# Performance work log

Measured on AMD Instinct MI355X. Metric: run time of the kernel, lower is better.

The kernel has to match this reference:

```python
import jax, jax.numpy as jnp
import numpy as np

H = 128
IN = 5
EPS = 1e-5


def lstm(x, Wih, Whh, bih, bhh):
    # x: [B,T,D]; PyTorch gate order i,f,g,o along 4H axis
    B, T, _ = x.shape
    xW = jnp.einsum('btd,gd->btg', x, Wih) + bih + bhh  # [B,T,4H]
    WhhT = Whh.T

    def step(carry, xt):
        h, c = carry
        g = xt + h @ WhhT
        i, f, gg, o = jnp.split(g, 4, axis=-1)
        i = jax.nn.sigmoid(i)
        f = jax.nn.sigmoid(f)
        gg = jnp.tanh(gg)
        o = jax.nn.sigmoid(o)
        c = f * c + i * gg
        h = o * jnp.tanh(c)
        return (h, c), h

    h0 = jnp.zeros((B, H), x.dtype)
    _, hs = jax.lax.scan(step, (h0, h0), jnp.swapaxes(xW, 0, 1))
    return jnp.swapaxes(hs, 0, 1)  # [B,T,H]


def batchnorm(x, gamma, beta):
    # training-mode BN over (batch, time) per channel; x: [B,T,H]
    mean = jnp.mean(x, axis=(0, 1))
    var = jnp.var(x, axis=(0, 1))
    return (x - mean) * (gamma * jax.lax.rsqrt(var + EPS)) + beta


def forward_one(x, Wih1, Whh1, bih1, bhh1, g1, b1, Wih2, Whh2, bih2, bhh2, g2, b2, fcW, fcb):
    out = lstm(x, Wih1, Whh1, bih1, bhh1)
    out = batchnorm(out, g1, b1)
    # dropout is identity (eval / deterministic reference)
    out = lstm(out, Wih2, Whh2, bih2, bhh2)
    out = batchnorm(out, g2, b2)
    emb = out[:, -1, :] @ fcW.T + fcb  # [B,128]
    norm = jnp.sqrt(jnp.sum(emb * emb, axis=1, keepdims=True))
    return emb / jnp.maximum(norm, 1e-12)  # F.normalize p=2


def setup_inputs() -> dict:
    key = jax.random.key(0)
    ks = jax.random.split(key, 20)
    B, T = 512, 128
    s_in = 1.0 / np.sqrt(H)
    d = {
        'a': jax.random.normal(ks[0], (B, T, IN), jnp.float32),
        'p': jax.random.normal(ks[1], (B, T, IN), jnp.float32),
        'n': jax.random.normal(ks[2], (B, T, IN), jnp.float32),
        'Wih1': jax.random.uniform(ks[3], (4 * H, IN), jnp.float32, -s_in, s_in),
        'Whh1': jax.random.uniform(ks[4], (4 * H, H), jnp.float32, -s_in, s_in),
        'bih1': jax.random.uniform(ks[5], (4 * H,), jnp.float32, -s_in, s_in),
        'bhh1': jax.random.uniform(ks[6], (4 * H,), jnp.float32, -s_in, s_in),
        'g1': jnp.ones((H,), jnp.float32),
        'b1': jnp.zeros((H,), jnp.float32),
        'Wih2': jax.random.uniform(ks[7], (4 * H, H), jnp.float32, -s_in, s_in),
        'Whh2': jax.random.uniform(ks[8], (4 * H, H), jnp.float32, -s_in, s_in),
        'bih2': jax.random.uniform(ks[9], (4 * H,), jnp.float32, -s_in, s_in),
        'bhh2': jax.random.uniform(ks[10], (4 * H,), jnp.float32, -s_in, s_in),
        'g2': jnp.ones((H,), jnp.float32),
        'b2': jnp.zeros((H,), jnp.float32),
        'fcW': jax.random.uniform(ks[11], (H, H), jnp.float32, -s_in, s_in),
        'fcb': jax.random.uniform(ks[12], (H,), jnp.float32, -s_in, s_in),
    }
    return d


def reference(a, p, n, Wih1, Whh1, bih1, bhh1, g1, b1, Wih2, Whh2, bih2, bhh2, g2, b2, fcW, fcb):
    f = lambda x: forward_one(x, Wih1, Whh1, bih1, bhh1, g1, b1, Wih2, Whh2, bih2, bhh2, g2, b2, fcW, fcb)
    return (f(a), f(p), f(n))
```

## Files before the change

### kernel.cpp

```cpp
#include <hip/hip_runtime.h>


typedef __attribute__((ext_vector_type(8))) _Float16 half8;
typedef __attribute__((ext_vector_type(4))) float f32x4;

#define TS 128
#define HID 128
#define NGATE 512
#define INV_N (1.0f/65536.0f)
#define NL2E  -1.4426950408889634f
#define N2L2E -2.8853900817779268f
#define GCLAMP 57.707801635558536f

#define BAR() asm volatile("s_waitcnt lgkmcnt(0)\n\ts_barrier" ::: "memory")

__device__ __forceinline__ float rcpf(float x) { return __builtin_amdgcn_rcpf(x); }
__device__ __forceinline__ float ex2(float x) { return __builtin_amdgcn_exp2f(x); }

__device__ __forceinline__ float lstm_cell(float zi, float zf, float zg, float zo,
                                           float& c) {
  float zgc = __builtin_amdgcn_fmed3f(zg, -GCLAMP, GCLAMP);
  float ei = ex2(zi);
  float ef = ex2(zf);
  float eg = ex2(zgc);
  float eo = ex2(zo);
  float pi = 1.0f + ei, pg = 1.0f + eg, pf = 1.0f + ef;
  float P = pi * pg;
  float rd = rcpf(P * pf);
  float fv = P * rd;
  float ig = (1.0f - eg) * (pf * rd);
  float cc = fv * c + ig;
  c = cc;
  float t2 = __builtin_amdgcn_fmed3f(cc * N2L2E, -GCLAMP, GCLAMP);
  float ec = ex2(t2);
  float hv = (1.0f - ec) * rcpf((1.0f + eo) * (1.0f + ec));
  return hv;
}


__global__ void prep_all(const float* __restrict__ xa, const float* __restrict__ xp,
                         const float* __restrict__ xn,
                         const float* __restrict__ Whh1, const float* __restrict__ Whh2,
                         const float* __restrict__ bih1, const float* __restrict__ bhh1,
                         _Float16* __restrict__ xpad,
                         _Float16* __restrict__ whhT1, _Float16* __restrict__ whhT2,
                         float* __restrict__ b1c) {
  int bid = blockIdx.x, tid = threadIdx.x;
  if (bid < 768) {
    int i = bid * 256 + tid;
    int tile = i >> 11, rem = i & 2047;
    int t = rem >> 4, r = rem & 15;
    int inp = tile >> 5, rloc = (tile & 31) * 16;
    const float* x = (inp == 0) ? xa : ((inp == 1) ? xp : xn);
    const float* row = x + (size_t)(rloc + r) * 640 + t * 5;
    half8 v = {0, 0, 0, 0, 0, 0, 0, 0};
#pragma unroll
    for (int j = 0; j < 5; ++j) v[j] = (_Float16)row[j];
    *(half8*)&xpad[(size_t)i * 8] = v;
  } else if (bid < 832) {
    int i = (bid - 768) * 256 + tid;
    int which = i >> 13, i8 = i & 8191;
    int kq = i8 >> 9, g = i8 & 511;
    int k0 = (kq >> 2) * 32 + (kq & 3) * 8;
    float gs = ((g >> 7) == 2) ? N2L2E : NL2E;
    const float* src = which ? Whh2 : Whh1;
    half8 v;
#pragma unroll
    for (int j = 0; j < 8; ++j) v[j] = (_Float16)(src[(size_t)g * HID + k0 + j] * gs);
    *(half8*)&(which ? whhT2 : whhT1)[(size_t)i8 * 8] = v;
  } else {
    int i = (bid - 832) * 256 + tid;
    float gs = ((i >> 7) == 2) ? N2L2E : NL2E;
    b1c[i] = (bih1[i] + bhh1[i]) * gs;
  }
}

__global__ __launch_bounds__(512, 2) void lstm1_kernel(
    const _Float16* __restrict__ xpad,
    const float* __restrict__ Wih1,
    const float* __restrict__ b1c,
    const _Float16* __restrict__ whhT,
    _Float16* __restrict__ hs1,
    float* __restrict__ s1sum, float* __restrict__ s1sq) {
  const int wg = blockIdx.x;
  const int inp = wg >> 5;
  const int tid = threadIdx.x;
  const int w = tid >> 6;
  const int lane = tid & 63;
  const int l15 = lane & 15;
  const int quad = lane >> 4;
  const int col = w * 16 + l15;

  __shared__ _Float16 hb[2][2048];
  for (int i = tid; i < 4096; i += 512) ((_Float16*)hb)[i] = (_Float16)0.0f;

  const int rbase = (quad * 16 + l15) * 8;
  const int wbase = (w >> 1) * 512 + ((w & 1) * 2 + (l15 >> 3)) * 128 +
                    quad * 32 + (l15 & 7);

  half8 bh[4][4];
#pragma unroll
  for (int kt = 0; kt < 4; ++kt)
#pragma unroll
    for (int gt = 0; gt < 4; ++gt)
      bh[kt][gt] = *(const half8*)&whhT[(size_t)((kt * 4 + quad) * 512 + gt * 128 + col) * 8];

  half8 bx[4];
#pragma unroll
  for (int gt = 0; gt < 4; ++gt) {
    half8 v = {0, 0, 0, 0, 0, 0, 0, 0};
    if (quad == 0) {
      float gs = (gt == 2) ? N2L2E : NL2E;
#pragma unroll
      for (int j = 0; j < 5; ++j) v[j] = (_Float16)(Wih1[(gt * 128 + col) * 5 + j] * gs);
    }
    bx[gt] = v;
  }
  f32x4 biasv[4];
#pragma unroll
  for (int gt = 0; gt < 4; ++gt) {
    float b = b1c[gt * 128 + col];
    biasv[gt][0] = b; biasv[gt][1] = b; biasv[gt][2] = b; biasv[gt][3] = b;
  }

  half8 xp = {0, 0, 0, 0, 0, 0, 0, 0};
  if (quad == 0) xp = *(const half8*)&xpad[((size_t)(wg * TS) * 16 + l15) * 8];

  float c[4] = {0, 0, 0, 0};
  float ssum = 0.0f, ssq = 0.0f;
  _Float16* hs1w = hs1 + (size_t)wg * TS * 2048;

  for (int t = 0; t < TS; ++t) {
    BAR();
    half8 ah[4];
#pragma unroll
    for (int kt = 0; kt < 4; ++kt)
      ah[kt] = *(const half8*)&hb[t & 1][kt * 512 + rbase];
    if (t > 0) {
      float2 cp = *(const float2*)&hb[t & 1][tid * 4];
      *(float2*)&hs1w[(size_t)(t - 1) * 2048 + tid * 4] = cp;
    }
    f32x4 acc[4];
#pragma unroll
    for (int gt = 0; gt < 4; ++gt)
      acc[gt] = __builtin_amdgcn_mfma_f32_16x16x32_f16(xp, bx[gt], biasv[gt], 0, 0, 0);
    if (t + 1 < TS && quad == 0)
      xp = *(const half8*)&xpad[((size_t)(wg * TS + t + 1) * 16 + l15) * 8];
#pragma unroll
    for (int kt = 0; kt < 4; ++kt)
#pragma unroll
      for (int gt = 0; gt < 4; ++gt)
        acc[gt] = __builtin_amdgcn_mfma_f32_16x16x32_f16(ah[kt], bh[kt][gt], acc[gt], 0, 0, 0);
    const int wb = (t + 1) & 1;
    float hv4[4];
#pragma unroll
    for (int r = 0; r < 4; ++r) {
      float hv = lstm_cell(acc[0][r], acc[1][r], acc[2][r], acc[3][r], c[r]);
      hb[wb][wbase + r * 8] = (_Float16)hv;
      hv4[r] = hv;
    }
#pragma unroll
    for (int r = 0; r < 4; ++r) { ssum += hv4[r]; ssq += hv4[r] * hv4[r]; }
  }
  BAR();
  {
    float2 cp = *(const float2*)&hb[0][tid * 4];
    *(float2*)&hs1w[(size_t)(TS - 1) * 2048 + tid * 4] = cp;
  }
  float s = ssum, q = ssq;
  s += __shfl_xor(s, 16); s += __shfl_xor(s, 32);
  q += __shfl_xor(q, 16); q += __shfl_xor(q, 32);
  if (quad == 0) {
    atomicAdd(&s1sum[inp * HID + col], s);
    atomicAdd(&s1sq[inp * HID + col], q);
  }
}

__global__ void mid_kernel(const float* __restrict__ s1sum, const float* __restrict__ s1sq,
                           const float* __restrict__ g1, const float* __restrict__ b1,
                           const float* __restrict__ Wih2,
                           const float* __restrict__ bih2, const float* __restrict__ bhh2,
                           _Float16* __restrict__ w2s, float* __restrict__ bias2eff) {
  int bid = blockIdx.x, tid = threadIdx.x;
  __shared__ float scB[8];
  __shared__ float shL[128];
  if (bid < 96) {
    int i = bid * 256 + tid;
    int inp = i >> 13, i8 = i & 8191;
    int kq = i8 >> 9, g = i8 & 511;
    int k0 = (kq >> 2) * 32 + (kq & 3) * 8;
    if (tid < 8) {
      int k = k0 + tid;
      float m = s1sum[inp * HID + k] * INV_N;
      float v = s1sq[inp * HID + k] * INV_N - m * m;
      scB[tid] = g1[k] * rsqrtf(v + 1e-5f);
    }
    __syncthreads();
    float gs = ((g >> 7) == 2) ? N2L2E : NL2E;
    const float* wr = Wih2 + (size_t)g * HID + k0;
    half8 v;
#pragma unroll
    for (int j = 0; j < 8; ++j) v[j] = (_Float16)(scB[j] * wr[j] * gs);
    *(half8*)&w2s[((size_t)inp * 8192 + i8) * 8] = v;
  } else {
    int i = (bid - 96) * 256 + tid;
    int inp = i >> 9, g = i & 511;
    if (tid < 128) {
      float m = s1sum[inp * HID + tid] * INV_N;
      float v = s1sq[inp * HID + tid] * INV_N - m * m;
      float s = g1[tid] * rsqrtf(v + 1e-5f);
      shL[tid] = b1[tid] - m * s;
    }
    __syncthreads();
    float acc = bih2[g] + bhh2[g];
    for (int h = 0; h < HID; ++h) acc += shL[h] * Wih2[(size_t)g * HID + h];
    float gs = ((g >> 7) == 2) ? N2L2E : NL2E;
    bias2eff[i] = acc * gs;
  }
}

__global__ __launch_bounds__(512, 2) void lstm2_kernel(
    const _Float16* __restrict__ hs1,
    const _Float16* __restrict__ whhT2,
    const _Float16* __restrict__ w2s,
    const float* __restrict__ bias2eff,
    _Float16* __restrict__ h_last,
    float* __restrict__ s2sum, float* __restrict__ s2sq) {
  const int wg = blockIdx.x;
  const int inp = wg >> 5;
  const int gr0 = wg * 16;
  const int tid = threadIdx.x;
  const int w = tid >> 6;
  const int lane = tid & 63;
  const int l15 = lane & 15;
  const int quad = lane >> 4;
  const int col = w * 16 + l15;

  __shared__ _Float16 hb[2][2048];
  for (int i = tid; i < 4096; i += 512) ((_Float16*)hb)[i] = (_Float16)0.0f;

  const int rbase = (quad * 16 + l15) * 8;
  const int wbase = (w >> 1) * 512 + ((w & 1) * 2 + (l15 >> 3)) * 128 +
                    quad * 32 + (l15 & 7);

  const _Float16* w2sI = w2s + (size_t)inp * HID * NGATE;
  half8 bh[4][4], bxw[4][4];
#pragma unroll
  for (int kt = 0; kt < 4; ++kt)
#pragma unroll
    for (int gt = 0; gt < 4; ++gt) {
      size_t gi = (size_t)((kt * 4 + quad) * 512 + gt * 128 + col) * 8;
      bh[kt][gt] = *(const half8*)&whhT2[gi];
      bxw[kt][gt] = *(const half8*)&w2sI[gi];
    }
  f32x4 biasv[4];
#pragma unroll
  for (int gt = 0; gt < 4; ++gt) {
    float b = bias2eff[inp * NGATE + gt * 128 + col];
    biasv[gt][0] = b; biasv[gt][1] = b; biasv[gt][2] = b; biasv[gt][3] = b;
  }

  const _Float16* hg = hs1 + (size_t)wg * TS * 2048;
  half8 a2A[4], a2B[4];
#pragma unroll
  for (int kt = 0; kt < 4; ++kt) {
    a2A[kt] = *(const half8*)&hg[kt * 512 + rbase];
    a2B[kt] = *(const half8*)&hg[(size_t)2048 + kt * 512 + rbase];
  }

  float c[4] = {0, 0, 0, 0};
  float ssum = 0.0f, ssq = 0.0f;

  auto step = [&](int t, half8 (&cur)[4]) {
    BAR();
    half8 ah[4];
#pragma unroll
    for (int kt = 0; kt < 4; ++kt)
      ah[kt] = *(const half8*)&hb[t & 1][kt * 512 + rbase];
    f32x4 acc[4];
#pragma unroll
    for (int gt = 0; gt < 4; ++gt)
      acc[gt] = __builtin_amdgcn_mfma_f32_16x16x32_f16(cur[0], bxw[0][gt], biasv[gt], 0, 0, 0);
#pragma unroll
    for (int kt = 1; kt < 4; ++kt)
#pragma unroll
      for (int gt = 0; gt < 4; ++gt)
        acc[gt] = __builtin_amdgcn_mfma_f32_16x16x32_f16(cur[kt], bxw[kt][gt], acc[gt], 0, 0, 0);
    if (t + 2 < TS) {
#pragma unroll
      for (int kt = 0; kt < 4; ++kt)
        cur[kt] = *(const half8*)&hg[(size_t)(t + 2) * 2048 + kt * 512 + rbase];
    }
#pragma unroll
    for (int kt = 0; kt < 4; ++kt)
#pragma unroll
      for (int gt = 0; gt < 4; ++gt)
        acc[gt] = __builtin_amdgcn_mfma_f32_16x16x32_f16(ah[kt], bh[kt][gt], acc[gt], 0, 0, 0);
    const int wb = (t + 1) & 1;
    float hv4[4];
#pragma unroll
    for (int r = 0; r < 4; ++r) {
      float hv = lstm_cell(acc[0][r], acc[1][r], acc[2][r], acc[3][r], c[r]);
      hb[wb][wbase + r * 8] = (_Float16)hv;
      hv4[r] = hv;
    }
#pragma unroll
    for (int r = 0; r < 4; ++r) { ssum += hv4[r]; ssq += hv4[r] * hv4[r]; }
  };

  for (int t = 0; t < TS; t += 2) {
    step(t, a2A);
    step(t + 1, a2B);
  }

  BAR();
#pragma unroll
  for (int r = 0; r < 4; ++r)
    h_last[(size_t)(gr0 + quad * 4 + r) * HID + col] = hb[0][wbase + r * 8];

  float s = ssum, q = ssq;
  s += __shfl_xor(s, 16); s += __shfl_xor(s, 32);
  q += __shfl_xor(q, 16); q += __shfl_xor(q, 32);
  if (quad == 0) {
    atomicAdd(&s2sum[inp * HID + col], s);
    atomicAdd(&s2sq[inp * HID + col], q);
  }
}

__global__ __launch_bounds__(256, 1) void head_kernel(
    const _Float16* __restrict__ h_last,
    const float* __restrict__ s2sum, const float* __restrict__ s2sq,
    const float* __restrict__ g2, const float* __restrict__ b2,
    const float* __restrict__ fcW, const float* __restrict__ fcb,
    float* __restrict__ out) {
  const int wg = blockIdx.x;
  const int inp = wg >> 5;
  const int gr0 = wg * 16;
  const int tid = threadIdx.x;

  __shared__ float fcwT[128][132];
  __shared__ float bnh[16][132];
  __shared__ float s2[128], sh2[128];
  __shared__ float part[16][16];
  __shared__ float inv[16];

  if (tid < 128) {
    float m = s2sum[inp * HID + tid] * INV_N;
    float v = s2sq[inp * HID + tid] * INV_N - m * m;
    float s = g2[tid] * rsqrtf(v + 1e-5f);
    s2[tid] = s; sh2[tid] = b2[tid] - m * s;
  }
  for (int i = tid; i < 16384; i += 256) {
    int j = i >> 7, h = i & 127;
    fcwT[h][j] = fcW[i];
  }
  __syncthreads();
  {
    int row = tid >> 4, c0 = (tid & 15) * 8;
#pragma unroll
    for (int k = 0; k < 8; ++k) {
      int h = c0 + k;
      bnh[row][h] = (float)h_last[(gr0 + row) * HID + h] * s2[h] + sh2[h];
    }
  }
  __syncthreads();
  const int row = tid >> 4, jl = tid & 15;
  float emb[8];
  float sq = 0.0f;
#pragma unroll
  for (int jj = 0; jj < 8; ++jj) {
    int j = jl + jj * 16;
    float acc = fcb[j];
    for (int h = 0; h < HID; ++h) acc += bnh[row][h] * fcwT[h][j];
    emb[jj] = acc; sq += acc * acc;
  }
  part[row][jl] = sq;
  __syncthreads();
  if (tid < 16) {
    float s = 0.0f;
    for (int k = 0; k < 16; ++k) s += part[tid][k];
    float nrm = sqrtf(s);
    inv[tid] = 1.0f / fmaxf(nrm, 1e-12f);
  }
  __syncthreads();
#pragma unroll
  for (int jj = 0; jj < 8; ++jj)
    out[(gr0 + row) * HID + jl + jj * 16] = emb[jj] * inv[row];
}

extern "C" void kernel_launch(void* const* d_in, const int* in_sizes, int n_in,
                              void* d_out, int out_size, void* d_ws, size_t ws_size,
                              hipStream_t stream) {
  const float* a    = (const float*)d_in[0];
  const float* p    = (const float*)d_in[1];
  const float* nn   = (const float*)d_in[2];
  const float* Wih1 = (const float*)d_in[3];
  const float* Whh1 = (const float*)d_in[4];
  const float* bih1 = (const float*)d_in[5];
  const float* bhh1 = (const float*)d_in[6];
  const float* g1   = (const float*)d_in[7];
  const float* b1   = (const float*)d_in[8];
  const float* Wih2 = (const float*)d_in[9];
  const float* Whh2 = (const float*)d_in[10];
  const float* bih2 = (const float*)d_in[11];
  const float* bhh2 = (const float*)d_in[12];
  const float* g2   = (const float*)d_in[13];
  const float* b2   = (const float*)d_in[14];
  const float* fcW  = (const float*)d_in[15];
  const float* fcb  = (const float*)d_in[16];

  char* ws = (char*)d_ws;
  float* s1sum = (float*)(ws + 0);
  float* s1sq  = s1sum + 384;
  float* s2sum = s1sum + 768;
  float* s2sq  = s1sum + 1152;
  float* b1c      = (float*)(ws + 6144);
  float* bias2eff = (float*)(ws + 8192);
  _Float16* whhT1 = (_Float16*)(ws + 14336);
  _Float16* whhT2 = (_Float16*)(ws + 145408);
  _Float16* w2s   = (_Float16*)(ws + 276480);
  _Float16* hlast = (_Float16*)(ws + 669696);
  _Float16* xpad  = (_Float16*)(ws + 1062912);
  _Float16* hs1   = (_Float16*)(ws + 4208640);

  hipMemsetAsync(ws, 0, 6144, stream);

  prep_all<<<834, 256, 0, stream>>>(a, p, nn, Whh1, Whh2, bih1, bhh1,
                                    xpad, whhT1, whhT2, b1c);
  lstm1_kernel<<<96, 512, 0, stream>>>(xpad, Wih1, b1c, whhT1, hs1, s1sum, s1sq);
  mid_kernel<<<102, 256, 0, stream>>>(s1sum, s1sq, g1, b1, Wih2, bih2, bhh2,
                                      w2s, bias2eff);
  lstm2_kernel<<<96, 512, 0, stream>>>(hs1, whhT2, w2s, bias2eff, hlast, s2sum, s2sq);
  head_kernel<<<96, 256, 0, stream>>>(hlast, s2sum, s2sq, g2, b2, fcW, fcb, (float*)d_out);
}
```

Measured before the change: 337.1 us.

## Fold prep and mid kernels into LSTM kernels and software-pipeline input projection

Removes the separate prep_all and mid_kernel launches. Each LSTM kernel now converts its own weights from fp32, computes the bias and batchnorm folding in its prologue, and lstm1 stages its input sequence into LDS. Both recurrent loops are software-pipelined: the input-projection MFMAs for step t+1 are issued after the recurrent MFMAs of step t, which takes them off the serial dependency chain. This saves two launches and several workspace round-trips, at the cost of redundant per-block weight conversion, a scalar bias dot product in every block, and 32KB of extra LDS in lstm1.

Result: slower. 390.0 us (+15.7%).

```diff
diff --git a/kernel.cpp b/kernel.cpp
--- a/kernel.cpp
+++ b/kernel.cpp
@@ -38,52 +38,17 @@
 }
 
 
-__global__ void prep_all(const float* __restrict__ xa, const float* __restrict__ xp,
-                         const float* __restrict__ xn,
-                         const float* __restrict__ Whh1, const float* __restrict__ Whh2,
-                         const float* __restrict__ bih1, const float* __restrict__ bhh1,
-                         _Float16* __restrict__ xpad,
-                         _Float16* __restrict__ whhT1, _Float16* __restrict__ whhT2,
-                         float* __restrict__ b1c) {
-  int bid = blockIdx.x, tid = threadIdx.x;
-  if (bid < 768) {
-    int i = bid * 256 + tid;
-    int tile = i >> 11, rem = i & 2047;
-    int t = rem >> 4, r = rem & 15;
-    int inp = tile >> 5, rloc = (tile & 31) * 16;
-    const float* x = (inp == 0) ? xa : ((inp == 1) ? xp : xn);
-    const float* row = x + (size_t)(rloc + r) * 640 + t * 5;
-    half8 v = {0, 0, 0, 0, 0, 0, 0, 0};
-#pragma unroll
-    for (int j = 0; j < 5; ++j) v[j] = (_Float16)row[j];
-    *(half8*)&xpad[(size_t)i * 8] = v;
-  } else if (bid < 832) {
-    int i = (bid - 768) * 256 + tid;
-    int which = i >> 13, i8 = i & 8191;
-    int kq = i8 >> 9, g = i8 & 511;
-    int k0 = (kq >> 2) * 32 + (kq & 3) * 8;
-    float gs = ((g >> 7) == 2) ? N2L2E : NL2E;
-    const float* src = which ? Whh2 : Whh1;
-    half8 v;
-#pragma unroll
-    for (int j = 0; j < 8; ++j) v[j] = (_Float16)(src[(size_t)g * HID + k0 + j] * gs);
-    *(half8*)&(which ? whhT2 : whhT1)[(size_t)i8 * 8] = v;
-  } else {
-    int i = (bid - 832) * 256 + tid;
-    float gs = ((i >> 7) == 2) ? N2L2E : NL2E;
-    b1c[i] = (bih1[i] + bhh1[i]) * gs;
-  }
-}
-
 __global__ __launch_bounds__(512, 2) void lstm1_kernel(
-    const _Float16* __restrict__ xpad,
+    const float* __restrict__ xa, const float* __restrict__ xpi,
+    const float* __restrict__ xn,
     const float* __restrict__ Wih1,
-    const float* __restrict__ b1c,
-    const _Float16* __restrict__ whhT,
+    const float* __restrict__ bih1, const float* __restrict__ bhh1,
+    const float* __restrict__ Whh1,
     _Float16* __restrict__ hs1,
     float* __restrict__ s1sum, float* __restrict__ s1sq) {
   const int wg = blockIdx.x;
   const int inp = wg >> 5;
+  const int rloc = (wg & 31) * 16;
   const int tid = threadIdx.x;
   const int w = tid >> 6;
   const int lane = tid & 63;
@@ -92,7 +57,19 @@
   const int col = w * 16 + l15;
 
   __shared__ _Float16 hb[2][2048];
-  for (int i = tid; i < 4096; i += 512) ((_Float16*)hb)[i] = (_Float16)0.0f;
+  __shared__ _Float16 xl[16384];
+
+  ((half8*)hb)[tid] = (half8){0, 0, 0, 0, 0, 0, 0, 0};
+  for (int i = tid; i < 2048; i += 512)
+    ((half8*)xl)[i] = (half8){0, 0, 0, 0, 0, 0, 0, 0};
+  __syncthreads();
+
+  const float* xg = (inp == 0) ? xa : ((inp == 1) ? xpi : xn);
+  for (int i = tid; i < 10240; i += 512) {
+    int r = i / 640, cc = i - r * 640;
+    int t = cc / 5, d = cc - t * 5;
+    xl[(t * 16 + r) * 8 + d] = (_Float16)xg[(size_t)(rloc + r) * 640 + cc];
+  }
 
   const int rbase = (quad * 16 + l15) * 8;
   const int wbase = (w >> 1) * 512 + ((w & 1) * 2 + (l15 >> 3)) * 128 +
@@ -102,9 +79,19 @@
 #pragma unroll
   for (int kt = 0; kt < 4; ++kt)
 #pragma unroll
-    for (int gt = 0; gt < 4; ++gt)
-      bh[kt][gt] = *(const half8*)&whhT[(size_t)((kt * 4 + quad) * 512 + gt * 128 + col) * 8];
-
+    for (int gt = 0; gt < 4; ++gt) {
+      int gcol = gt * 128 + col;
+      float gs = (gt == 2) ? N2L2E : NL2E;
+      const float* ph = Whh1 + (size_t)gcol * HID + kt * 32 + quad * 8;
+      f32x4 h0 = *(const f32x4*)ph, h1 = *(const f32x4*)(ph + 4);
+      half8 v;
+#pragma unroll
+      for (int j = 0; j < 4; ++j) {
+        v[j] = (_Float16)(h0[j] * gs);
+        v[4 + j] = (_Float16)(h1[j] * gs);
+      }
+      bh[kt][gt] = v;
+    }
   half8 bx[4];
 #pragma unroll
   for (int gt = 0; gt < 4; ++gt) {
@@ -112,55 +99,67 @@
     if (quad == 0) {
       float gs = (gt == 2) ? N2L2E : NL2E;
 #pragma unroll
-      for (int j = 0; j < 5; ++j) v[j] = (_Float16)(Wih1[(gt * 128 + col) * 5 + j] * gs);
+      for (int j = 0; j < 5; ++j)
+        v[j] = (_Float16)(Wih1[(gt * 128 + col) * 5 + j] * gs);
     }
     bx[gt] = v;
   }
   f32x4 biasv[4];
 #pragma unroll
   for (int gt = 0; gt < 4; ++gt) {
-    float b = b1c[gt * 128 + col];
+    int gcol = gt * 128 + col;
+    float gs = (gt == 2) ? N2L2E : NL2E;
+    float b = (bih1[gcol] + bhh1[gcol]) * gs;
     biasv[gt][0] = b; biasv[gt][1] = b; biasv[gt][2] = b; biasv[gt][3] = b;
   }
 
-  half8 xp = {0, 0, 0, 0, 0, 0, 0, 0};
-  if (quad == 0) xp = *(const half8*)&xpad[((size_t)(wg * TS) * 16 + l15) * 8];
-
-  float c[4] = {0, 0, 0, 0};
+  __syncthreads();
+
+  half8 xp0 = *(const half8*)&xl[l15 * 8];
+  f32x4 accA[4], accB[4];
+#pragma unroll
+  for (int gt = 0; gt < 4; ++gt)
+    accA[gt] = __builtin_amdgcn_mfma_f32_16x16x32_f16(xp0, bx[gt], biasv[gt], 0, 0, 0);
+
+  float c4[4] = {0, 0, 0, 0};
   float ssum = 0.0f, ssq = 0.0f;
   _Float16* hs1w = hs1 + (size_t)wg * TS * 2048;
 
-  for (int t = 0; t < TS; ++t) {
+  auto step = [&](int t, f32x4 (&aC)[4], f32x4 (&aN)[4]) {
     BAR();
     half8 ah[4];
 #pragma unroll
     for (int kt = 0; kt < 4; ++kt)
       ah[kt] = *(const half8*)&hb[t & 1][kt * 512 + rbase];
+    int tn = (t + 1 < TS) ? t + 1 : TS - 1;
+    half8 xpn = *(const half8*)&xl[(tn * 16 + l15) * 8];
     if (t > 0) {
       float2 cp = *(const float2*)&hb[t & 1][tid * 4];
       *(float2*)&hs1w[(size_t)(t - 1) * 2048 + tid * 4] = cp;
     }
-    f32x4 acc[4];
+#pragma unroll
+    for (int kt = 0; kt < 4; ++kt)
+#pragma unroll
+      for (int gt = 0; gt < 4; ++gt)
+        aC[gt] = __builtin_amdgcn_mfma_f32_16x16x32_f16(ah[kt], bh[kt][gt], aC[gt], 0, 0, 0);
 #pragma unroll
     for (int gt = 0; gt < 4; ++gt)
-      acc[gt] = __builtin_amdgcn_mfma_f32_16x16x32_f16(xp, bx[gt], biasv[gt], 0, 0, 0);
-    if (t + 1 < TS && quad == 0)
-      xp = *(const half8*)&xpad[((size_t)(wg * TS + t + 1) * 16 + l15) * 8];
-#pragma unroll
-    for (int kt = 0; kt < 4; ++kt)
-#pragma unroll
-      for (int gt = 0; gt < 4; ++gt)
-        acc[gt] = __builtin_amdgcn_mfma_f32_16x16x32_f16(ah[kt], bh[kt][gt], acc[gt], 0, 0, 0);
+      aN[gt] = __builtin_amdgcn_mfma_f32_16x16x32_f16(xpn, bx[gt], biasv[gt], 0, 0, 0);
     const int wb = (t + 1) & 1;
     float hv4[4];
 #pragma unroll
     for (int r = 0; r < 4; ++r) {
-      float hv = lstm_cell(acc[0][r], acc[1][r], acc[2][r], acc[3][r], c[r]);
+      float hv = lstm_cell(aC[0][r], aC[1][r], aC[2][r], aC[3][r], c4[r]);
       hb[wb][wbase + r * 8] = (_Float16)hv;
       hv4[r] = hv;
     }
 #pragma unroll
     for (int r = 0; r < 4; ++r) { ssum += hv4[r]; ssq += hv4[r] * hv4[r]; }
+  };
+
+  for (int t = 0; t < TS; t += 2) {
+    step(t, accA, accB);
+    step(t + 1, accB, accA);
   }
   BAR();
   {
@@ -176,54 +175,13 @@
   }
 }
 
-__global__ void mid_kernel(const float* __restrict__ s1sum, const float* __restrict__ s1sq,
-                           const float* __restrict__ g1, const float* __restrict__ b1,
-                           const float* __restrict__ Wih2,
-                           const float* __restrict__ bih2, const float* __restrict__ bhh2,
-                           _Float16* __restrict__ w2s, float* __restrict__ bias2eff) {
-  int bid = blockIdx.x, tid = threadIdx.x;
-  __shared__ float scB[8];
-  __shared__ float shL[128];
-  if (bid < 96) {
-    int i = bid * 256 + tid;
-    int inp = i >> 13, i8 = i & 8191;
-    int kq = i8 >> 9, g = i8 & 511;
-    int k0 = (kq >> 2) * 32 + (kq & 3) * 8;
-    if (tid < 8) {
-      int k = k0 + tid;
-      float m = s1sum[inp * HID + k] * INV_N;
-      float v = s1sq[inp * HID + k] * INV_N - m * m;
-      scB[tid] = g1[k] * rsqrtf(v + 1e-5f);
-    }
-    __syncthreads();
-    float gs = ((g >> 7) == 2) ? N2L2E : NL2E;
-    const float* wr = Wih2 + (size_t)g * HID + k0;
-    half8 v;
-#pragma unroll
-    for (int j = 0; j < 8; ++j) v[j] = (_Float16)(scB[j] * wr[j] * gs);
-    *(half8*)&w2s[((size_t)inp * 8192 + i8) * 8] = v;
-  } else {
-    int i = (bid - 96) * 256 + tid;
-    int inp = i >> 9, g = i & 511;
-    if (tid < 128) {
-      float m = s1sum[inp * HID + tid] * INV_N;
-      float v = s1sq[inp * HID + tid] * INV_N - m * m;
-      float s = g1[tid] * rsqrtf(v + 1e-5f);
-      shL[tid] = b1[tid] - m * s;
-    }
-    __syncthreads();
-    float acc = bih2[g] + bhh2[g];
-    for (int h = 0; h < HID; ++h) acc += shL[h] * Wih2[(size_t)g * HID + h];
-    float gs = ((g >> 7) == 2) ? N2L2E : NL2E;
-    bias2eff[i] = acc * gs;
-  }
-}
-
 __global__ __launch_bounds__(512, 2) void lstm2_kernel(
     const _Float16* __restrict__ hs1,
-    const _Float16* __restrict__ whhT2,
-    const _Float16* __restrict__ w2s,
-    const float* __restrict__ bias2eff,
+    const float* __restrict__ Whh2,
+    const float* __restrict__ Wih2,
+    const float* __restrict__ bih2, const float* __restrict__ bhh2,
+    const float* __restrict__ g1, const float* __restrict__ b1,
+    const float* __restrict__ s1sum, const float* __restrict__ s1sq,
     _Float16* __restrict__ h_last,
     float* __restrict__ s2sum, float* __restrict__ s2sq) {
   const int wg = blockIdx.x;
@@ -237,26 +195,58 @@
   const int col = w * 16 + l15;
 
   __shared__ _Float16 hb[2][2048];
-  for (int i = tid; i < 4096; i += 512) ((_Float16*)hb)[i] = (_Float16)0.0f;
+  __shared__ float scb[128], shb[128];
+
+  ((half8*)hb)[tid] = (half8){0, 0, 0, 0, 0, 0, 0, 0};
+  if (tid < 128) {
+    float m = s1sum[inp * HID + tid] * INV_N;
+    float v = s1sq[inp * HID + tid] * INV_N - m * m;
+    float s = g1[tid] * rsqrtf(v + 1e-5f);
+    scb[tid] = s;
+    shb[tid] = b1[tid] - m * s;
+  }
+  __syncthreads();
 
   const int rbase = (quad * 16 + l15) * 8;
   const int wbase = (w >> 1) * 512 + ((w & 1) * 2 + (l15 >> 3)) * 128 +
                     quad * 32 + (l15 & 7);
 
-  const _Float16* w2sI = w2s + (size_t)inp * HID * NGATE;
   half8 bh[4][4], bxw[4][4];
 #pragma unroll
   for (int kt = 0; kt < 4; ++kt)
 #pragma unroll
     for (int gt = 0; gt < 4; ++gt) {
-      size_t gi = (size_t)((kt * 4 + quad) * 512 + gt * 128 + col) * 8;
-      bh[kt][gt] = *(const half8*)&whhT2[gi];
-      bxw[kt][gt] = *(const half8*)&w2sI[gi];
+      int gcol = gt * 128 + col;
+      float gs = (gt == 2) ? N2L2E : NL2E;
+      int k0 = kt * 32 + quad * 8;
+      const float* ph = Whh2 + (size_t)gcol * HID + k0;
+      const float* px = Wih2 + (size_t)gcol * HID + k0;
+      f32x4 h0 = *(const f32x4*)ph, h1 = *(const f32x4*)(ph + 4);
+      f32x4 x0 = *(const f32x4*)px, x1 = *(const f32x4*)(px + 4);
+      half8 vh, vx;
+#pragma unroll
+      for (int j = 0; j < 4; ++j) {
+        vh[j] = (_Float16)(h0[j] * gs);
+        vh[4 + j] = (_Float16)(h1[j] * gs);
+        vx[j] = (_Float16)(x0[j] * scb[k0 + j] * gs);
+        vx[4 + j] = (_Float16)(x1[j] * scb[k0 + 4 + j] * gs);
+      }
+      bh[kt][gt] = vh;
+      bxw[kt][gt] = vx;
     }
   f32x4 biasv[4];
 #pragma unroll
   for (int gt = 0; gt < 4; ++gt) {
-    float b = bias2eff[inp * NGATE + gt * 128 + col];
+    int gcol = gt * 128 + col;
+    float gs = (gt == 2) ? N2L2E : NL2E;
+    float b = bih2[gcol] + bhh2[gcol];
+    const float* pr = Wih2 + (size_t)gcol * HID;
+    for (int h0 = 0; h0 < HID; h0 += 4) {
+      f32x4 wv = *(const f32x4*)&pr[h0];
+      b += shb[h0] * wv[0] + shb[h0 + 1] * wv[1] +
+           shb[h0 + 2] * wv[2] + shb[h0 + 3] * wv[3];
+    }
+    b *= gs;
     biasv[gt][0] = b; biasv[gt][1] = b; biasv[gt][2] = b; biasv[gt][3] = b;
   }
 
@@ -267,40 +257,49 @@
     a2A[kt] = *(const half8*)&hg[kt * 512 + rbase];
     a2B[kt] = *(const half8*)&hg[(size_t)2048 + kt * 512 + rbase];
   }
-
-  float c[4] = {0, 0, 0, 0};
+  f32x4 accA[4], accB[4];
+#pragma unroll
+  for (int gt = 0; gt < 4; ++gt)
+    accA[gt] = __builtin_amdgcn_mfma_f32_16x16x32_f16(a2A[0], bxw[0][gt], biasv[gt], 0, 0, 0);
+#pragma unroll
+  for (int kt = 1; kt < 4; ++kt)
+#pragma unroll
+    for (int gt = 0; gt < 4; ++gt)
+      accA[gt] = __builtin_amdgcn_mfma_f32_16x16x32_f16(a2A[kt], bxw[kt][gt], accA[gt], 0, 0, 0);
+
+  float c4[4] = {0, 0, 0, 0};
   float ssum = 0.0f, ssq = 0.0f;
 
-  auto step = [&](int t, half8 (&cur)[4]) {
+  auto step = [&](int t, f32x4 (&aC)[4], f32x4 (&aN)[4],
+                  half8 (&fT)[4], half8 (&fS)[4]) {
     BAR();
     half8 ah[4];
 #pragma unroll
     for (int kt = 0; kt < 4; ++kt)
       ah[kt] = *(const half8*)&hb[t & 1][kt * 512 + rbase];
-    f32x4 acc[4];
+#pragma unroll
+    for (int kt = 0; kt < 4; ++kt)
+#pragma unroll
+      for (int gt = 0; gt < 4; ++gt)
+        aC[gt] = __builtin_amdgcn_mfma_f32_16x16x32_f16(ah[kt], bh[kt][gt], aC[gt], 0, 0, 0);
+    if (t + 2 < TS) {
+#pragma unroll
+      for (int kt = 0; kt < 4; ++kt)
+        fT[kt] = *(const half8*)&hg[(size_t)(t + 2) * 2048 + kt * 512 + rbase];
+    }
 #pragma unroll
     for (int gt = 0; gt < 4; ++gt)
-      acc[gt] = __builtin_amdgcn_mfma_f32_16x16x32_f16(cur[0], bxw[0][gt], biasv[gt], 0, 0, 0);
+      aN[gt] = __builtin_amdgcn_mfma_f32_16x16x32_f16(fS[0], bxw[0][gt], biasv[gt], 0, 0, 0);
 #pragma unroll
     for (int kt = 1; kt < 4; ++kt)
 #pragma unroll
       for (int gt = 0; gt < 4; ++gt)
-        acc[gt] = __builtin_amdgcn_mfma_f32_16x16x32_f16(cur[kt], bxw[kt][gt], acc[gt], 0, 0, 0);
-    if (t + 2 < TS) {
-#pragma unroll
-      for (int kt = 0; kt < 4; ++kt)
-        cur[kt] = *(const half8*)&hg[(size_t)(t + 2) * 2048 + kt * 512 + rbase];
-    }
-#pragma unroll
-    for (int kt = 0; kt < 4; ++kt)
-#pragma unroll
-      for (int gt = 0; gt < 4; ++gt)
-        acc[gt] = __builtin_amdgcn_mfma_f32_16x16x32_f16(ah[kt], bh[kt][gt], acc[gt], 0, 0, 0);
+        aN[gt] = __builtin_amdgcn_mfma_f32_16x16x32_f16(fS[kt], bxw[kt][gt], aN[gt], 0, 0, 0);
     const int wb = (t + 1) & 1;
     float hv4[4];
 #pragma unroll
     for (int r = 0; r < 4; ++r) {
-      float hv = lstm_cell(acc[0][r], acc[1][r], acc[2][r], acc[3][r], c[r]);
+      float hv = lstm_cell(aC[0][r], aC[1][r], aC[2][r], aC[3][r], c4[r]);
       hb[wb][wbase + r * 8] = (_Float16)hv;
       hv4[r] = hv;
     }
@@ -309,8 +308,8 @@
   };
 
   for (int t = 0; t < TS; t += 2) {
-    step(t, a2A);
-    step(t + 1, a2B);
+    step(t, accA, accB, a2A, a2B);
+    step(t + 1, accB, accA, a2B, a2A);
   }
 
   BAR();
@@ -414,22 +413,15 @@
   float* s1sq  = s1sum + 384;
   float* s2sum = s1sum + 768;
   float* s2sq  = s1sum + 1152;
-  float* b1c      = (float*)(ws + 6144);
-  float* bias2eff = (float*)(ws + 8192);
-  _Float16* whhT1 = (_Float16*)(ws + 14336);
-  _Float16* whhT2 = (_Float16*)(ws + 145408);
-  _Float16* w2s   = (_Float16*)(ws + 276480);
-  _Float16* hlast = (_Float16*)(ws + 669696);
-  _Float16* xpad  = (_Float16*)(ws + 1062912);
-  _Float16* hs1   = (_Float16*)(ws + 4208640);
+  _Float16* hlast = (_Float16*)(ws + 6144);
+  _Float16* hs1   = (_Float16*)(ws + 399360);
 
   hipMemsetAsync(ws, 0, 6144, stream);
 
-  prep_all<<<834, 256, 0, stream>>>(a, p, nn, Whh1, Whh2, bih1, bhh1,
-                                    xpad, whhT1, whhT2, b1c);
-  lstm1_kernel<<<96, 512, 0, stream>>>(xpad, Wih1, b1c, whhT1, hs1, s1sum, s1sq);
-  mid_kernel<<<102, 256, 0, stream>>>(s1sum, s1sq, g1, b1, Wih2, bih2, bhh2,
-                                      w2s, bias2eff);
-  lstm2_kernel<<<96, 512, 0, stream>>>(hs1, whhT2, w2s, bias2eff, hlast, s2sum, s2sq);
-  head_kernel<<<96, 256, 0, stream>>>(hlast, s2sum, s2sq, g2, b2, fcW, fcb, (float*)d_out);
+  lstm1_kernel<<<96, 512, 0, stream>>>(a, p, nn, Wih1, bih1, bhh1, Whh1,
+                                       hs1, s1sum, s1sq);
+  lstm2_kernel<<<96, 512, 0, stream>>>(hs1, Whh2, Wih2, bih2, bhh2, g1, b1,
+                                       s1sum, s1sq, hlast, s2sum, s2sq);
+  head_kernel<<<96, 256, 0, stream>>>(hlast, s2sum, s2sq, g2, b2, fcW, fcb,
+                                      (float*)d_out);
 }
```

## Interleave two independent batch tiles per workgroup in layer-2 LSTM recurrence

Applied to the files above, without the earlier changes.

Each lstm2 workgroup now processes two 16-row batch tiles (A and B) staggered by half a step, so tile B's MFMA work overlaps tile A's gate math and barrier latency, and the reverse. The grid is halved from 96 to 48 workgroups, with twice the LDS state per block. This targets latency in the serial recurrence, but uses half as many CUs and adds register pressure from the doubled accumulators and carried state.

Result: slower. 512.7 us (+52.1%).

```diff
diff --git a/kernel.cpp b/kernel.cpp
--- a/kernel.cpp
+++ b/kernel.cpp
@@ -227,8 +227,8 @@
     _Float16* __restrict__ h_last,
     float* __restrict__ s2sum, float* __restrict__ s2sq) {
   const int wg = blockIdx.x;
-  const int inp = wg >> 5;
-  const int gr0 = wg * 16;
+  const int tA = wg * 2, tB = tA + 1;
+  const int inp = tA >> 5;
   const int tid = threadIdx.x;
   const int w = tid >> 6;
   const int lane = tid & 63;
@@ -236,8 +236,11 @@
   const int quad = lane >> 4;
   const int col = w * 16 + l15;
 
-  __shared__ _Float16 hb[2][2048];
-  for (int i = tid; i < 4096; i += 512) ((_Float16*)hb)[i] = (_Float16)0.0f;
+  __shared__ _Float16 hbA[2][2048];
+  __shared__ _Float16 hbB[2][2048];
+
+  ((half8*)hbA)[tid] = (half8){0, 0, 0, 0, 0, 0, 0, 0};
+  ((half8*)hbB)[tid] = (half8){0, 0, 0, 0, 0, 0, 0, 0};
 
   const int rbase = (quad * 16 + l15) * 8;
   const int wbase = (w >> 1) * 512 + ((w & 1) * 2 + (l15 >> 3)) * 128 +
@@ -260,63 +263,113 @@
     biasv[gt][0] = b; biasv[gt][1] = b; biasv[gt][2] = b; biasv[gt][3] = b;
   }
 
-  const _Float16* hg = hs1 + (size_t)wg * TS * 2048;
-  half8 a2A[4], a2B[4];
+  const _Float16* hgA = hs1 + (size_t)tA * TS * 2048;
+  const _Float16* hgB = hs1 + (size_t)tB * TS * 2048;
+
+  half8 fA[4], fB[4];
+#pragma unroll
+  for (int kt = 0; kt < 4; ++kt) fA[kt] = *(const half8*)&hgA[kt * 512 + rbase];
+
+  f32x4 accA[4], accB[4];
+#pragma unroll
+  for (int gt = 0; gt < 4; ++gt)
+    accA[gt] = __builtin_amdgcn_mfma_f32_16x16x32_f16(fA[0], bxw[0][gt], biasv[gt], 0, 0, 0);
+#pragma unroll
+  for (int kt = 1; kt < 4; ++kt)
+#pragma unroll
+    for (int gt = 0; gt < 4; ++gt)
+      accA[gt] = __builtin_amdgcn_mfma_f32_16x16x32_f16(fA[kt], bxw[kt][gt], accA[gt], 0, 0, 0);
 #pragma unroll
   for (int kt = 0; kt < 4; ++kt) {
-    a2A[kt] = *(const half8*)&hg[kt * 512 + rbase];
-    a2B[kt] = *(const half8*)&hg[(size_t)2048 + kt * 512 + rbase];
-  }
-
-  float c[4] = {0, 0, 0, 0};
+    fB[kt] = *(const half8*)&hgB[kt * 512 + rbase];
+    fA[kt] = *(const half8*)&hgA[(size_t)2048 + kt * 512 + rbase];
+  }
+
+  float cA[4] = {0, 0, 0, 0}, cB[4] = {0, 0, 0, 0};
   float ssum = 0.0f, ssq = 0.0f;
 
-  auto step = [&](int t, half8 (&cur)[4]) {
+  __syncthreads();
+
+  for (int t = 0; t < TS; ++t) {
+    half8 ahA[4];
+#pragma unroll
+    for (int kt = 0; kt < 4; ++kt)
+      ahA[kt] = *(const half8*)&hbA[t & 1][kt * 512 + rbase];
+    if (t > 0) {
+#pragma unroll
+      for (int r = 0; r < 4; ++r) {
+        float hv = lstm_cell(accB[0][r], accB[1][r], accB[2][r], accB[3][r], cB[r]);
+        hbB[t & 1][wbase + r * 8] = (_Float16)hv;
+        ssum += hv; ssq += hv * hv;
+      }
+    }
+#pragma unroll
+    for (int gt = 0; gt < 4; ++gt)
+      accB[gt] = __builtin_amdgcn_mfma_f32_16x16x32_f16(fB[0], bxw[0][gt], biasv[gt], 0, 0, 0);
+#pragma unroll
+    for (int kt = 1; kt < 4; ++kt)
+#pragma unroll
+      for (int gt = 0; gt < 4; ++gt)
+        accB[gt] = __builtin_amdgcn_mfma_f32_16x16x32_f16(fB[kt], bxw[kt][gt], accB[gt], 0, 0, 0);
+    {
+      int tn = (t + 1 < TS) ? t + 1 : TS - 1;
+#pragma unroll
+      for (int kt = 0; kt < 4; ++kt)
+        fB[kt] = *(const half8*)&hgB[(size_t)tn * 2048 + kt * 512 + rbase];
+    }
+#pragma unroll
+    for (int kt = 0; kt < 4; ++kt)
+#pragma unroll
+      for (int gt = 0; gt < 4; ++gt)
+        accA[gt] = __builtin_amdgcn_mfma_f32_16x16x32_f16(ahA[kt], bh[kt][gt], accA[gt], 0, 0, 0);
     BAR();
-    half8 ah[4];
-#pragma unroll
-    for (int kt = 0; kt < 4; ++kt)
-      ah[kt] = *(const half8*)&hb[t & 1][kt * 512 + rbase];
-    f32x4 acc[4];
+    half8 ahB[4];
+#pragma unroll
+    for (int kt = 0; kt < 4; ++kt)
+      ahB[kt] = *(const half8*)&hbB[t & 1][kt * 512 + rbase];
+    {
+      const int wb = (t + 1) & 1;
+#pragma unroll
+      for (int r = 0; r < 4; ++r) {
+        float hv = lstm_cell(accA[0][r], accA[1][r], accA[2][r], accA[3][r], cA[r]);
+        hbA[wb][wbase + r * 8] = (_Float16)hv;
+        ssum += hv; ssq += hv * hv;
+      }
+    }
 #pragma unroll
     for (int gt = 0; gt < 4; ++gt)
-      acc[gt] = __builtin_amdgcn_mfma_f32_16x16x32_f16(cur[0], bxw[0][gt], biasv[gt], 0, 0, 0);
+      accA[gt] = __builtin_amdgcn_mfma_f32_16x16x32_f16(fA[0], bxw[0][gt], biasv[gt], 0, 0, 0);
 #pragma unroll
     for (int kt = 1; kt < 4; ++kt)
 #pragma unroll
       for (int gt = 0; gt < 4; ++gt)
-        acc[gt] = __builtin_amdgcn_mfma_f32_16x16x32_f16(cur[kt], bxw[kt][gt], acc[gt], 0, 0, 0);
-    if (t + 2 < TS) {
+        accA[gt] = __builtin_amdgcn_mfma_f32_16x16x32_f16(fA[kt], bxw[kt][gt], accA[gt], 0, 0, 0);
+    {
+      int tn = (t + 2 < TS) ? t + 2 : TS - 1;
 #pragma unroll
       for (int kt = 0; kt < 4; ++kt)
-        cur[kt] = *(const half8*)&hg[(size_t)(t + 2) * 2048 + kt * 512 + rbase];
+        fA[kt] = *(const half8*)&hgA[(size_t)tn * 2048 + kt * 512 + rbase];
     }
 #pragma unroll
     for (int kt = 0; kt < 4; ++kt)
 #pragma unroll
       for (int gt = 0; gt < 4; ++gt)
-        acc[gt] = __builtin_amdgcn_mfma_f32_16x16x32_f16(ah[kt], bh[kt][gt], acc[gt], 0, 0, 0);
-    const int wb = (t + 1) & 1;
-    float hv4[4];
-#pragma unroll
-    for (int r = 0; r < 4; ++r) {
-      float hv = lstm_cell(acc[0][r], acc[1][r], acc[2][r], acc[3][r], c[r]);
-      hb[wb][wbase + r * 8] = (_Float16)hv;
-      hv4[r] = hv;
-    }
-#pragma unroll
-    for (int r = 0; r < 4; ++r) { ssum += hv4[r]; ssq += hv4[r] * hv4[r]; }
-  };
-
-  for (int t = 0; t < TS; t += 2) {
-    step(t, a2A);
-    step(t + 1, a2B);
-  }
-
+        accB[gt] = __builtin_amdgcn_mfma_f32_16x16x32_f16(ahB[kt], bh[kt][gt], accB[gt], 0, 0, 0);
+    BAR();
+  }
+
+#pragma unroll
+  for (int r = 0; r < 4; ++r) {
+    float hv = lstm_cell(accB[0][r], accB[1][r], accB[2][r], accB[3][r], cB[r]);
+    hbB[0][wbase + r * 8] = (_Float16)hv;
+    ssum += hv; ssq += hv * hv;
+  }
   BAR();
 #pragma unroll
-  for (int r = 0; r < 4; ++r)
-    h_last[(size_t)(gr0 + quad * 4 + r) * HID + col] = hb[0][wbase + r * 8];
+  for (int r = 0; r < 4; ++r) {
+    h_last[(size_t)(tA * 16 + quad * 4 + r) * HID + col] = hbA[0][wbase + r * 8];
+    h_last[(size_t)(tB * 16 + quad * 4 + r) * HID + col] = hbB[0][wbase + r * 8];
+  }
 
   float s = ssum, q = ssq;
   s += __shfl_xor(s, 16); s += __shfl_xor(s, 32);
@@ -430,6 +483,6 @@
   lstm1_kernel<<<96, 512, 0, stream>>>(xpad, Wih1, b1c, whhT1, hs1, s1sum, s1sq);
   mid_kernel<<<102, 256, 0, stream>>>(s1sum, s1sq, g1, b1, Wih2, bih2, bhh2,
                                       w2s, bias2eff);
-  lstm2_kernel<<<96, 512, 0, stream>>>(hs1, whhT2, w2s, bias2eff, hlast, s2sum, s2sq);
+  lstm2_kernel<<<48, 512, 0, stream>>>(hs1, whhT2, w2s, bias2eff, hlast, s2sum, s2sq);
   head_kernel<<<96, 256, 0, stream>>>(hlast, s2sum, s2sq, g2, b2, fcW, fcb, (float*)d_out);
 }
```

## Interleave two batch tiles per workgroup in LSTM1 and fold stats memset into prep

Applied to the files above, without the earlier changes.

Each lstm1 workgroup now processes two independent 16-row batch tiles in lockstep, halving the grid to 48 workgroups. The two recurrences interleave their MFMA chains and gate math so each hides the other's dependency latency within a barrier step. The hipMemsetAsync is replaced by an extra prep block that zeroes the stats buffer, and lstm2 writes h_last inside the final step instead of after a trailing barrier. The cost is more registers and LDS per workgroup, and fewer workgroups, so only 48 CUs are used for layer 1.

After: 434.8 us. 29.0% more time.

```diff
diff --git a/kernel.cpp b/kernel.cpp
--- a/kernel.cpp
+++ b/kernel.cpp
@@ -44,7 +44,7 @@
                          const float* __restrict__ bih1, const float* __restrict__ bhh1,
                          _Float16* __restrict__ xpad,
                          _Float16* __restrict__ whhT1, _Float16* __restrict__ whhT2,
-                         float* __restrict__ b1c) {
+                         float* __restrict__ b1c, float* __restrict__ stats) {
   int bid = blockIdx.x, tid = threadIdx.x;
   if (bid < 768) {
     int i = bid * 256 + tid;
@@ -68,10 +68,13 @@
 #pragma unroll
     for (int j = 0; j < 8; ++j) v[j] = (_Float16)(src[(size_t)g * HID + k0 + j] * gs);
     *(half8*)&(which ? whhT2 : whhT1)[(size_t)i8 * 8] = v;
-  } else {
+  } else if (bid < 834) {
     int i = (bid - 832) * 256 + tid;
     float gs = ((i >> 7) == 2) ? N2L2E : NL2E;
     b1c[i] = (bih1[i] + bhh1[i]) * gs;
+  } else {
+#pragma unroll
+    for (int j = 0; j < 6; ++j) stats[tid * 6 + j] = 0.0f;
   }
 }
 
@@ -83,7 +86,8 @@
     _Float16* __restrict__ hs1,
     float* __restrict__ s1sum, float* __restrict__ s1sq) {
   const int wg = blockIdx.x;
-  const int inp = wg >> 5;
+  const int tA = wg * 2, tB = tA + 1;
+  const int inp = tA >> 5;
   const int tid = threadIdx.x;
   const int w = tid >> 6;
   const int lane = tid & 63;
@@ -91,8 +95,8 @@
   const int quad = lane >> 4;
   const int col = w * 16 + l15;
 
-  __shared__ _Float16 hb[2][2048];
-  for (int i = tid; i < 4096; i += 512) ((_Float16*)hb)[i] = (_Float16)0.0f;
+  __shared__ _Float16 hb[2][2][2048];
+  for (int i = tid; i < 8192; i += 512) ((_Float16*)hb)[i] = (_Float16)0.0f;
 
   const int rbase = (quad * 16 + l15) * 8;
   const int wbase = (w >> 1) * 512 + ((w & 1) * 2 + (l15 >> 3)) * 128 +
@@ -123,49 +127,66 @@
     biasv[gt][0] = b; biasv[gt][1] = b; biasv[gt][2] = b; biasv[gt][3] = b;
   }
 
-  half8 xp = {0, 0, 0, 0, 0, 0, 0, 0};
-  if (quad == 0) xp = *(const half8*)&xpad[((size_t)(wg * TS) * 16 + l15) * 8];
-
-  float c[4] = {0, 0, 0, 0};
+  half8 xpA = {0, 0, 0, 0, 0, 0, 0, 0};
+  half8 xpB = {0, 0, 0, 0, 0, 0, 0, 0};
+  if (quad == 0) {
+    xpA = *(const half8*)&xpad[((size_t)(tA * TS) * 16 + l15) * 8];
+    xpB = *(const half8*)&xpad[((size_t)(tB * TS) * 16 + l15) * 8];
+  }
+
+  float cA[4] = {0, 0, 0, 0}, cB[4] = {0, 0, 0, 0};
   float ssum = 0.0f, ssq = 0.0f;
-  _Float16* hs1w = hs1 + (size_t)wg * TS * 2048;
+  _Float16* hsA = hs1 + (size_t)tA * TS * 2048;
+  _Float16* hsB = hs1 + (size_t)tB * TS * 2048;
 
   for (int t = 0; t < TS; ++t) {
     BAR();
-    half8 ah[4];
+    half8 ahA[4], ahB[4];
+#pragma unroll
+    for (int kt = 0; kt < 4; ++kt) {
+      ahA[kt] = *(const half8*)&hb[0][t & 1][kt * 512 + rbase];
+      ahB[kt] = *(const half8*)&hb[1][t & 1][kt * 512 + rbase];
+    }
+    if (t > 0) {
+      float2 cpA = *(const float2*)&hb[0][t & 1][tid * 4];
+      *(float2*)&hsA[(size_t)(t - 1) * 2048 + tid * 4] = cpA;
+      float2 cpB = *(const float2*)&hb[1][t & 1][tid * 4];
+      *(float2*)&hsB[(size_t)(t - 1) * 2048 + tid * 4] = cpB;
+    }
+    f32x4 accA[4], accB[4];
+#pragma unroll
+    for (int gt = 0; gt < 4; ++gt) {
+      accA[gt] = __builtin_amdgcn_mfma_f32_16x16x32_f16(xpA, bx[gt], biasv[gt], 0, 0, 0);
+      accB[gt] = __builtin_amdgcn_mfma_f32_16x16x32_f16(xpB, bx[gt], biasv[gt], 0, 0, 0);
+    }
+    if (t + 1 < TS && quad == 0) {
+      xpA = *(const half8*)&xpad[((size_t)(tA * TS + t + 1) * 16 + l15) * 8];
+      xpB = *(const half8*)&xpad[((size_t)(tB * TS + t + 1) * 16 + l15) * 8];
+    }
 #pragma unroll
     for (int kt = 0; kt < 4; ++kt)
-      ah[kt] = *(const half8*)&hb[t & 1][kt * 512 + rbase];
-    if (t > 0) {
-      float2 cp = *(const float2*)&hb[t & 1][tid * 4];
-      *(float2*)&hs1w[(size_t)(t - 1) * 2048 + tid * 4] = cp;
-    }
-    f32x4 acc[4];
-#pragma unroll
-    for (int gt = 0; gt < 4; ++gt)
-      acc[gt] = __builtin_amdgcn_mfma_f32_16x16x32_f16(xp, bx[gt], biasv[gt], 0, 0, 0);
-    if (t + 1 < TS && quad == 0)
-      xp = *(const half8*)&xpad[((size_t)(wg * TS + t + 1) * 16 + l15) * 8];
-#pragma unroll
-    for (int kt = 0; kt < 4; ++kt)
-#pragma unroll
-      for (int gt = 0; gt < 4; ++gt)
-        acc[gt] = __builtin_amdgcn_mfma_f32_16x16x32_f16(ah[kt], bh[kt][gt], acc[gt], 0, 0, 0);
+#pragma unroll
+      for (int gt = 0; gt < 4; ++gt) {
+        accA[gt] = __builtin_amdgcn_mfma_f32_16x16x32_f16(ahA[kt], bh[kt][gt], accA[gt], 0, 0, 0);
+        accB[gt] = __builtin_amdgcn_mfma_f32_16x16x32_f16(ahB[kt], bh[kt][gt], accB[gt], 0, 0, 0);
+      }
     const int wb = (t + 1) & 1;
-    float hv4[4];
 #pragma unroll
     for (int r = 0; r < 4; ++r) {
-      float hv = lstm_cell(acc[0][r], acc[1][r], acc[2][r], acc[3][r], c[r]);
-      hb[wb][wbase + r * 8] = (_Float16)hv;
-      hv4[r] = hv;
-    }
-#pragma unroll
-    for (int r = 0; r < 4; ++r) { ssum += hv4[r]; ssq += hv4[r] * hv4[r]; }
+      float hvA = lstm_cell(accA[0][r], accA[1][r], accA[2][r], accA[3][r], cA[r]);
+      float hvB = lstm_cell(accB[0][r], accB[1][r], accB[2][r], accB[3][r], cB[r]);
+      hb[0][wb][wbase + r * 8] = (_Float16)hvA;
+      hb[1][wb][wbase + r * 8] = (_Float16)hvB;
+      ssum += hvA + hvB;
+      ssq += hvA * hvA + hvB * hvB;
+    }
   }
   BAR();
   {
-    float2 cp = *(const float2*)&hb[0][tid * 4];
-    *(float2*)&hs1w[(size_t)(TS - 1) * 2048 + tid * 4] = cp;
+    float2 cpA = *(const float2*)&hb[0][0][tid * 4];
+    *(float2*)&hsA[(size_t)(TS - 1) * 2048 + tid * 4] = cpA;
+    float2 cpB = *(const float2*)&hb[1][0][tid * 4];
+    *(float2*)&hsB[(size_t)(TS - 1) * 2048 + tid * 4] = cpB;
   }
   float s = ssum, q = ssq;
   s += __shfl_xor(s, 16); s += __shfl_xor(s, 32);
@@ -301,8 +322,10 @@
 #pragma unroll
     for (int r = 0; r < 4; ++r) {
       float hv = lstm_cell(acc[0][r], acc[1][r], acc[2][r], acc[3][r], c[r]);
-      hb[wb][wbase + r * 8] = (_Float16)hv;
+      _Float16 hh = (_Float16)hv;
+      hb[wb][wbase + r * 8] = hh;
       hv4[r] = hv;
+      if (t == TS - 1) h_last[(size_t)(gr0 + quad * 4 + r) * HID + col] = hh;
     }
 #pragma unroll
     for (int r = 0; r < 4; ++r) { ssum += hv4[r]; ssq += hv4[r] * hv4[r]; }
@@ -312,11 +335,6 @@
     step(t, a2A);
     step(t + 1, a2B);
   }
-
-  BAR();
-#pragma unroll
-  for (int r = 0; r < 4; ++r)
-    h_last[(size_t)(gr0 + quad * 4 + r) * HID + col] = hb[0][wbase + r * 8];
 
   float s = ssum, q = ssq;
   s += __shfl_xor(s, 16); s += __shfl_xor(s, 32);
@@ -423,11 +441,9 @@
   _Float16* xpad  = (_Float16*)(ws + 1062912);
   _Float16* hs1   = (_Float16*)(ws + 4208640);
 
-  hipMemsetAsync(ws, 0, 6144, stream);
-
-  prep_all<<<834, 256, 0, stream>>>(a, p, nn, Whh1, Whh2, bih1, bhh1,
-                                    xpad, whhT1, whhT2, b1c);
-  lstm1_kernel<<<96, 512, 0, stream>>>(xpad, Wih1, b1c, whhT1, hs1, s1sum, s1sq);
+  prep_all<<<835, 256, 0, stream>>>(a, p, nn, Whh1, Whh2, bih1, bhh1,
+                                    xpad, whhT1, whhT2, b1c, s1sum);
+  lstm1_kernel<<<48, 512, 0, stream>>>(xpad, Wih1, b1c, whhT1, hs1, s1sum, s1sq);
   mid_kernel<<<102, 256, 0, stream>>>(s1sum, s1sq, g1, b1, Wih2, bih2, bhh2,
                                       w2s, bias2eff);
   lstm2_kernel<<<96, 512, 0, stream>>>(hs1, whhT2, w2s, bias2eff, hlast, s2sum, s2sq);
```
